# Kernel optimization log

Hardware: AMD Instinct MI355X
Metric: run time of the kernel (lower is better)

## Reference

```python
import jax, jax.numpy as jnp
import numpy as np

N = 50000        # nodes
N_EDGES = 800000 # edges before self loops
D_IN = 128       # in_features
D_OUT = 64       # out_features (per head)
H = 2            # heads
NEG_SLOPE = 0.2  # GATv2Conv default negative_slope
EPS = 1e-5       # LayerNorm eps


def setup_inputs() -> dict:
    key = jax.random.key(0)
    ks = jax.random.split(key, 8)
    X = jax.random.normal(ks[0], (N, D_IN), jnp.float32)
    E = jax.random.randint(ks[1], (2, N_EDGES), 0, N, dtype=jnp.int32)
    attr = jax.random.normal(ks[2], (N_EDGES,), jnp.float32)
    # GATv2Conv params: lin_l / lin_r (share_weights=False, bias=True), att, concat bias
    s_in = 1.0 / np.sqrt(D_IN)
    W_l = jax.random.normal(ks[3], (D_IN, H * D_OUT), jnp.float32) * s_in
    b_l = jnp.zeros((H * D_OUT,), jnp.float32)
    W_r = jax.random.normal(ks[4], (D_IN, H * D_OUT), jnp.float32) * s_in
    b_r = jnp.zeros((H * D_OUT,), jnp.float32)
    att = jax.random.normal(ks[5], (H, D_OUT), jnp.float32) * (1.0 / np.sqrt(D_OUT))
    bias = jnp.zeros((H * D_OUT,), jnp.float32)
    # final_linear + LayerNorm params
    W_f = jax.random.normal(ks[6], (H * D_OUT, D_OUT), jnp.float32) * (1.0 / np.sqrt(H * D_OUT))
    b_f = jnp.zeros((D_OUT,), jnp.float32)
    gamma = jnp.ones((D_OUT,), jnp.float32)
    beta = jnp.zeros((D_OUT,), jnp.float32)
    return dict(X=X, E=E, attr=attr, W_l=W_l, b_l=b_l, W_r=W_r, b_r=b_r,
                att=att, bias=bias, W_f=W_f, b_f=b_f, gamma=gamma, beta=beta)


def _forward(X, E, W_l, b_l, W_r, b_r, att, bias, W_f, b_f, gamma, beta):
    # add self loops (PyG GATv2Conv default add_self_loops=True)
    loop = jnp.arange(N, dtype=E.dtype)
    src = jnp.concatenate([E[0], loop])  # [Et]
    dst = jnp.concatenate([E[1], loop])  # [Et]
    x_l = (X @ W_l + b_l).reshape(N, H, D_OUT)  # source-side transform
    x_r = (X @ W_r + b_r).reshape(N, H, D_OUT)  # target-side transform
    # per-edge GATv2 score: a^T LeakyReLU(x_i + x_j)
    s = jax.nn.leaky_relu(x_l[src] + x_r[dst], NEG_SLOPE)      # [Et, H, C]
    alpha = jnp.einsum('ehc,hc->eh', s, att)                   # [Et, H]
    # segment softmax over incoming edges of each target node
    a_max = jax.ops.segment_max(alpha, dst, num_segments=N)    # [N, H]
    a_max = jnp.where(jnp.isfinite(a_max), a_max, 0.0)
    num = jnp.exp(alpha - a_max[dst])
    den = jax.ops.segment_sum(num, dst, num_segments=N)
    w = num / den[dst]                                         # [Et, H]
    # weighted scatter-aggregate of source messages
    out = jax.ops.segment_sum(x_l[src] * w[:, :, None], dst, num_segments=N)  # [N,H,C]
    out = out.reshape(N, H * D_OUT) + bias                     # concat heads + bias
    # final linear + LayerNorm
    h = out @ W_f + b_f                                        # [N, D_OUT]
    mu = jnp.mean(h, axis=-1, keepdims=True)
    var = jnp.mean((h - mu) ** 2, axis=-1, keepdims=True)
    return (h - mu) * jax.lax.rsqrt(var + EPS) * gamma + beta


def reference(X, E, attr, W_l, b_l, W_r, b_r, att, bias, W_f, b_f, gamma, beta):
    H_out = _forward(X, E, W_l, b_l, W_r, b_r, att, bias, W_f, b_f, gamma, beta)
    return (H_out, E, attr)
```

## Files before the change

kernel.cpp:

```cpp
#include <hip/hip_runtime.h>

typedef unsigned short u16;
typedef unsigned int   u32;


#define DIN   128
#define DOUT  64
#define HD    128
#define BCAP  64

typedef __attribute__((ext_vector_type(8))) _Float16 f16x8;
typedef __attribute__((ext_vector_type(2))) _Float16 h2;
typedef __attribute__((ext_vector_type(4))) float    f32x4;

union H2U { u32 u; h2 h; };
__device__ __forceinline__ h2  U2H(u32 u) { H2U x; x.u = u; return x.h; }
__device__ __forceinline__ u32 H2Ub(h2 h) { H2U x; x.h = h; return x.u; }

__device__ __forceinline__ u16 f2h(float f) {
    _Float16 h = (_Float16)f;
    u16 r; __builtin_memcpy(&r, &h, 2); return r;
}

__device__ __forceinline__ u32 pkmax(u32 a, u32 b) {
    u32 d;
    asm("v_pk_max_f16 %0, %1, %2" : "=v"(d) : "v"(a), "v"(b));
    return d;
}

__device__ __forceinline__ float fdot2f(h2 a, h2 b, float c) {
#if __has_builtin(__builtin_amdgcn_fdot2)
    return __builtin_amdgcn_fdot2(a, b, c, false);
#else
    return c + (float)a[0] * (float)b[0] + (float)a[1] * (float)b[1];
#endif
}

__global__ void prep_small(const float* __restrict__ Wl, const float* __restrict__ Wr,
                           const float* __restrict__ Wf,
                           u16* __restrict__ WTl, u16* __restrict__ WTr,
                           uint4* __restrict__ Wfp, int* __restrict__ count, int N)
{
    int i = blockIdx.x * 256 + threadIdx.x;
    if (i < N) { count[i] = 0; return; }
    int j = i - N;
    if (j < 16384) {
        int k = j >> 7, c = j & 127;
        WTl[c * 128 + k] = f2h(Wl[j]);
    } else if (j < 32768) {
        int t = j - 16384;
        int k = t >> 7, c = t & 127;
        WTr[c * 128 + k] = f2h(Wr[t]);
    } else if (j < 33792) {
        int t = j - 32768;
        int k4 = t >> 5, c = t & 31;
        const float* wrow = Wf + (size_t)(4 * k4) * DOUT;
        u32 a0 = (u32)f2h(wrow[c])              | ((u32)f2h(wrow[DOUT + c]) << 16);
        u32 a1 = (u32)f2h(wrow[2 * DOUT + c])   | ((u32)f2h(wrow[3 * DOUT + c]) << 16);
        u32 a2 = (u32)f2h(wrow[c + 32])         | ((u32)f2h(wrow[DOUT + c + 32]) << 16);
        u32 a3 = (u32)f2h(wrow[2 * DOUT + c + 32]) | ((u32)f2h(wrow[3 * DOUT + c + 32]) << 16);
        Wfp[t] = make_uint4(a0, a1, a2, a3);
    }
}

__global__ __launch_bounds__(256) void gemm_scatter(
    const float* __restrict__ X,
    const u16* __restrict__ WTl, const float* __restrict__ bl,
    const u16* __restrict__ WTr, const float* __restrict__ br,
    const int* __restrict__ E, const float* __restrict__ attr,
    int* __restrict__ count, u16* __restrict__ bucket,
    u16* __restrict__ xl_p, u16* __restrict__ xr_p,
    float* __restrict__ out, int N, int NE)
{
    __shared__ u16 sX[64 * 136];
    __shared__ u16 sW[128 * 136];

    const int tid  = threadIdx.x;
    const int bid  = blockIdx.x;
    const int nB   = gridDim.x;
    const int cb   = bid & 1;
    const int row0 = (bid >> 1) * 64;
    const u16*   WT  = (cb == 0) ? WTl : WTr;
    const float* bia = (cb == 0) ? bl : br;

    {
        int e0 = (int)(((long long)bid) * NE / nB);
        int e1 = (int)(((long long)bid + 1) * NE / nB);
        for (int e = e0 + tid; e < e1; e += 256) {
            int src = E[e];
            int dst = E[NE + e];
            if ((u32)dst >= (u32)N) dst = 0;
            if ((u32)src >= (u32)N) src = 0;
            int rank = atomicAdd(&count[dst], 1);
            if (rank < BCAP) bucket[(size_t)dst * BCAP + rank] = (u16)src;
        }
        const size_t base = (size_t)N * DOUT;
        long long P = 3LL * NE;
        int p0 = (int)(((long long)bid) * P / nB);
        int p1 = (int)(((long long)bid + 1) * P / nB);
        for (int p = p0 + tid; p < p1; p += 256) {
            if (p < 2 * NE) out[base + p] = (float)E[p];
            else            out[base + p] = attr[p - 2 * NE];
        }
    }

    for (int idx = tid; idx < 64 * 32; idx += 256) {
        int r  = idx >> 5;
        int k4 = (idx & 31) << 2;
        int gr = row0 + r;
        float4 v = make_float4(0.f, 0.f, 0.f, 0.f);
        if (gr < N) v = *(const float4*)(X + (size_t)gr * DIN + k4);
        u32 p0 = (u32)f2h(v.x) | ((u32)f2h(v.y) << 16);
        u32 p1 = (u32)f2h(v.z) | ((u32)f2h(v.w) << 16);
        *(uint2*)&sX[r * 136 + k4] = make_uint2(p0, p1);
    }
    for (int idx = tid; idx < 128 * 16; idx += 256) {
        int c  = idx >> 4;
        int k8 = (idx & 15) << 3;
        *(uint4*)&sW[c * 136 + k8] = *(const uint4*)&WT[c * 128 + k8];
    }
    __syncthreads();

    const int wv   = tid >> 6;
    const int lane = tid & 63;
    const int m    = lane & 15;
    const int quad = lane >> 4;

    f32x4 acc[8] = {};
    #pragma unroll
    for (int kc = 0; kc < 4; kc++) {
        f16x8 bx = *(const f16x8*)&sX[(wv * 16 + m) * 136 + kc * 32 + quad * 8];
        #pragma unroll
        for (int t = 0; t < 8; t++) {
            f16x8 aw = *(const f16x8*)&sW[(t * 16 + m) * 136 + kc * 32 + quad * 8];
            acc[t] = __builtin_amdgcn_mfma_f32_16x16x32_f16(aw, bx, acc[t], 0, 0, 0);
        }
    }

    const int gn = row0 + wv * 16 + m;
    if (gn < N) {
        u16* dst = (cb == 0) ? xl_p : xr_p;
        #pragma unroll
        for (int t = 0; t < 8; t++) {
            const int c0 = t * 16 + quad * 4;
            float4 bv = *(const float4*)(bia + c0);
            u32 p0 = (u32)f2h(acc[t][0] + bv.x) | ((u32)f2h(acc[t][1] + bv.y) << 16);
            u32 p1 = (u32)f2h(acc[t][2] + bv.z) | ((u32)f2h(acc[t][3] + bv.w) << 16);
            *(uint2*)(dst + (size_t)gn * HD + c0) = make_uint2(p0, p1);
        }
    }
}

template<int D>
__device__ __forceinline__ void edge_block(
    int myidx, int j, int sgbase, const char* xbase,
    const h2* xr2, const h2* at2, h2 c02,
    h2* acc2, float& lden)
{
    uint4 q[D];
    #pragma unroll
    for (int b = 0; b < D; b++) {
        u32 off = (u32)__shfl(myidx, sgbase + j + 2 * b) << 8;
        q[b] = *(const uint4*)(xbase + off);
    }
    float sh[D];
    #pragma unroll
    for (int b = 0; b < D; b++) {
        h2 v0 = U2H(q[b].x) + xr2[0];
        h2 v1 = U2H(q[b].y) + xr2[1];
        h2 v2 = U2H(q[b].z) + xr2[2];
        h2 v3 = U2H(q[b].w) + xr2[3];
        v0 = U2H(pkmax(H2Ub(v0), H2Ub(v0 * c02)));
        v1 = U2H(pkmax(H2Ub(v1), H2Ub(v1 * c02)));
        v2 = U2H(pkmax(H2Ub(v2), H2Ub(v2 * c02)));
        v3 = U2H(pkmax(H2Ub(v3), H2Ub(v3 * c02)));
        float s = fdot2f(v0, at2[0], 0.f);
        s = fdot2f(v1, at2[1], s);
        s = fdot2f(v2, at2[2], s);
        s = fdot2f(v3, at2[3], s);
        sh[b] = s;
    }
    #pragma unroll
    for (int m = 4; m; m >>= 1) {
        #pragma unroll
        for (int b = 0; b < D; b++) sh[b] += __shfl_xor(sh[b], m);
    }
    #pragma unroll
    for (int b = 0; b < D; b++) {
        float p = exp2f(sh[b]);
        lden += p;
        _Float16 ph = (_Float16)p;
        h2 p2 = {ph, ph};
        acc2[0] += p2 * U2H(q[b].x);
        acc2[1] += p2 * U2H(q[b].y);
        acc2[2] += p2 * U2H(q[b].z);
        acc2[3] += p2 * U2H(q[b].w);
    }
}

__global__ __launch_bounds__(256, 6) void edge_fused(
    const u16* __restrict__ xl_p, const u16* __restrict__ xr_p,
    const float* __restrict__ att, const float* __restrict__ bias,
    const uint4* __restrict__ Wfp, const float* __restrict__ bf,
    const float* __restrict__ gamma, const float* __restrict__ beta,
    const int* __restrict__ count, const u16* __restrict__ bucket,
    float* __restrict__ out, int N)
{
    __shared__ uint4 sWp[32 * 32];
    __shared__ u32   sAggU[8 * 64];

    const int tid = threadIdx.x;
    for (int idx = tid; idx < 1024; idx += 256) sWp[idx] = Wfp[idx];
    __syncthreads();

    const int l      = tid & 63;
    const int half   = tid >> 5;
    const int hl     = tid & 31;
    const int g16    = l & 15;
    const int ch0    = g16 * 8;
    const int sgsel  = (l >> 4) & 1;
    const int sgbase = (l & 32) + sgsel;
    const int n      = blockIdx.x * 8 + half;
    const bool active = (n < N);

    const h2 c02 = {(_Float16)0.2f, (_Float16)0.2f};
    h2 at2[4], xr2[4];
    {
        const float L2E = 1.44269504f;
        float4 a0 = *(const float4*)(att + ch0);
        float4 a1 = *(const float4*)(att + ch0 + 4);
        at2[0] = h2{(_Float16)(a0.x * L2E), (_Float16)(a0.y * L2E)};
        at2[1] = h2{(_Float16)(a0.z * L2E), (_Float16)(a0.w * L2E)};
        at2[2] = h2{(_Float16)(a1.x * L2E), (_Float16)(a1.y * L2E)};
        at2[3] = h2{(_Float16)(a1.z * L2E), (_Float16)(a1.w * L2E)};
        uint4 pr = make_uint4(0, 0, 0, 0);
        if (active) pr = *(const uint4*)(xr_p + (size_t)n * HD + ch0);
        xr2[0] = U2H(pr.x); xr2[1] = U2H(pr.y);
        xr2[2] = U2H(pr.z); xr2[3] = U2H(pr.w);
    }

    h2 acc2[4] = {};
    float lden = 0.f;

    int cnt_b = 0;
    if (active) {
        cnt_b = count[n];
        if (cnt_b < 0) cnt_b = 0;
        if (cnt_b > BCAP) cnt_b = BCAP;
    }
    const int cnt = active ? cnt_b + 1 : 0;
    const u16* mybkt = bucket + (size_t)(active ? n : 0) * BCAP;

    const char* xbase = (const char*)xl_p + ch0 * 2;

    int done = 0;
    while (done < cnt) {
        int chunk = cnt - done; if (chunk > 32) chunk = 32;
        int myidx = 0;
        if (hl < chunk) {
            int gj = done + hl;
            myidx = (gj < cnt_b) ? (int)mybkt[gj] : n;
        }
        int j = 0;
        for (; j + 16 <= chunk; j += 16)
            edge_block<8>(myidx, j, sgbase, xbase, xr2, at2, c02, acc2, lden);
        if (j + 8 <= chunk) {
            edge_block<4>(myidx, j, sgbase, xbase, xr2, at2, c02, acc2, lden);
            j += 8;
        }
        if (j + 4 <= chunk) {
            edge_block<2>(myidx, j, sgbase, xbase, xr2, at2, c02, acc2, lden);
            j += 4;
        }
        for (; j < chunk; j += 2) {
            u32 off = (u32)__shfl(myidx, sgbase + j) << 8;
            uint4 q = *(const uint4*)(xbase + off);
            h2 v0 = U2H(q.x) + xr2[0];
            h2 v1 = U2H(q.y) + xr2[1];
            h2 v2 = U2H(q.z) + xr2[2];
            h2 v3 = U2H(q.w) + xr2[3];
            v0 = U2H(pkmax(H2Ub(v0), H2Ub(v0 * c02)));
            v1 = U2H(pkmax(H2Ub(v1), H2Ub(v1 * c02)));
            v2 = U2H(pkmax(H2Ub(v2), H2Ub(v2 * c02)));
            v3 = U2H(pkmax(H2Ub(v3), H2Ub(v3 * c02)));
            float s = fdot2f(v0, at2[0], 0.f);
            s = fdot2f(v1, at2[1], s);
            s = fdot2f(v2, at2[2], s);
            s = fdot2f(v3, at2[3], s);
            #pragma unroll
            for (int m = 4; m; m >>= 1) s += __shfl_xor(s, m);
            float p = (j + sgsel < chunk) ? exp2f(s) : 0.f;
            lden += p;
            _Float16 ph = (_Float16)p;
            h2 p2 = {ph, ph};
            acc2[0] += p2 * U2H(q.x);
            acc2[1] += p2 * U2H(q.y);
            acc2[2] += p2 * U2H(q.z);
            acc2[3] += p2 * U2H(q.w);
        }
        done += chunk;
    }

    #pragma unroll
    for (int i = 0; i < 4; i++) {
        u32 o = (u32)__shfl_xor((int)H2Ub(acc2[i]), 16);
        acc2[i] = acc2[i] + U2H(o);
    }
    lden += __shfl_xor(lden, 16);

    float rl = 1.f / fmaxf(lden, 1e-30f);
    if (!(l & 16)) {
        float4 b0 = *(const float4*)(bias + ch0);
        float4 b1 = *(const float4*)(bias + ch0 + 4);
        uint4 w;
        w.x = (u32)f2h((float)acc2[0][0] * rl + b0.x) |
              ((u32)f2h((float)acc2[0][1] * rl + b0.y) << 16);
        w.y = (u32)f2h((float)acc2[1][0] * rl + b0.z) |
              ((u32)f2h((float)acc2[1][1] * rl + b0.w) << 16);
        w.z = (u32)f2h((float)acc2[2][0] * rl + b1.x) |
              ((u32)f2h((float)acc2[2][1] * rl + b1.y) << 16);
        w.w = (u32)f2h((float)acc2[3][0] * rl + b1.z) |
              ((u32)f2h((float)acc2[3][1] * rl + b1.w) << 16);
        *(uint4*)&sAggU[half * 64 + g16 * 4] = w;
    }
    asm volatile("s_waitcnt lgkmcnt(0)" ::: "memory");

    float h0 = bf[hl], h1 = bf[hl + 32];
    #pragma unroll 8
    for (int k4 = 0; k4 < 32; k4++) {
        uint4 wp = sWp[k4 * 32 + hl];
        uint2 ag = *(const uint2*)&sAggU[half * 64 + k4 * 2];
        h0 = fdot2f(U2H(ag.x), U2H(wp.x), h0);
        h0 = fdot2f(U2H(ag.y), U2H(wp.y), h0);
        h1 = fdot2f(U2H(ag.x), U2H(wp.z), h1);
        h1 = fdot2f(U2H(ag.y), U2H(wp.w), h1);
    }

    float s1r = h0 + h1, s2r = h0 * h0 + h1 * h1;
    #pragma unroll
    for (int m = 16; m; m >>= 1) { s1r += __shfl_xor(s1r, m); s2r += __shfl_xor(s2r, m); }
    float mu  = s1r * (1.f / 64.f);
    float var = s2r * (1.f / 64.f) - mu * mu;
    float rs  = rsqrtf(fmaxf(var, 0.f) + 1e-5f);
    if (active) {
        out[(size_t)n * DOUT + hl]      = (h0 - mu) * rs * gamma[hl]      + beta[hl];
        out[(size_t)n * DOUT + hl + 32] = (h1 - mu) * rs * gamma[hl + 32] + beta[hl + 32];
    }
}

extern "C" void kernel_launch(void* const* d_in, const int* in_sizes, int n_in,
                              void* d_out, int out_size, void* d_ws, size_t ws_size,
                              hipStream_t stream) {
    const float* X    = (const float*)d_in[0];
    const int*   E    = (const int*)d_in[1];
    const float* attr = (const float*)d_in[2];
    const float* Wl   = (const float*)d_in[3];
    const float* bl   = (const float*)d_in[4];
    const float* Wr   = (const float*)d_in[5];
    const float* br   = (const float*)d_in[6];
    const float* att  = (const float*)d_in[7];
    const float* bias = (const float*)d_in[8];
    const float* Wf   = (const float*)d_in[9];
    const float* bf   = (const float*)d_in[10];
    const float* gamma= (const float*)d_in[11];
    const float* beta = (const float*)d_in[12];
    float* out = (float*)d_out;

    const int N  = in_sizes[0] / DIN;
    const int NE = in_sizes[1] / 2;
    const int GB = (N + 63) / 64;

    char* ws = (char*)d_ws;
    int* count      = (int*)ws;               ws += (size_t)N * 4;
    u16* bucket     = (u16*)ws;               ws += (size_t)N * BCAP * 2;
    u16* xl_p       = (u16*)ws;               ws += (size_t)N * HD * 2;
    u16* xr_p       = (u16*)ws;               ws += (size_t)N * HD * 2;
    u16* WTl        = (u16*)ws;               ws += 128 * 128 * 2;
    u16* WTr        = (u16*)ws;               ws += 128 * 128 * 2;
    uint4* Wfp      = (uint4*)ws;             ws += 1024 * 16;

    prep_small<<<(N + 33792 + 255) / 256, 256, 0, stream>>>(
        Wl, Wr, Wf, WTl, WTr, Wfp, count, N);

    gemm_scatter<<<2 * GB, 256, 0, stream>>>(
        X, WTl, bl, WTr, br, E, attr, count, bucket, xl_p, xr_p, out, N, NE);

    edge_fused<<<(N + 7) / 8, 256, 0, stream>>>(
        xl_p, xr_p, att, bias, Wfp, bf, gamma, beta,
        count, bucket, out, N);
}
```

Measured before the change: 215.8 us.

## Fuse all stages into one persistent cooperative kernel with grid syncs

Replaces the three kernel launches with a single persistent cooperative kernel sized to occupancy. The prep, GEMM/scatter and edge-aggregation stages are separated by grid-wide syncs. The GEMM now reads weights directly from global memory instead of staging them in LDS, and shared memory is overlaid through a union. Odd and even blocks order the GEMM and scatter work differently so the atomics overlap with MFMA work. This removes launch gaps and tail effects, at the risk of lower occupancy in the edge phase and the cost of the grid barriers. A three-kernel fallback is kept in case the cooperative launch fails.

```diff
diff --git a/kernel.cpp b/kernel.cpp
--- a/kernel.cpp
+++ b/kernel.cpp
@@ -1,4 +1,7 @@
 #include <hip/hip_runtime.h>
+#include <hip/hip_cooperative_groups.h>
+
+namespace cg = cooperative_groups;
 
 typedef unsigned short u16;
 typedef unsigned int   u32;
@@ -36,12 +39,16 @@
 #endif
 }
 
-__global__ void prep_small(const float* __restrict__ Wl, const float* __restrict__ Wr,
-                           const float* __restrict__ Wf,
-                           u16* __restrict__ WTl, u16* __restrict__ WTr,
-                           uint4* __restrict__ Wfp, int* __restrict__ count, int N)
-{
-    int i = blockIdx.x * 256 + threadIdx.x;
+union SharedU {
+    u16 sX[64 * 136];
+    struct { uint4 sWp[1024]; u32 sAggU[8 * 64]; } ef;
+};
+
+__device__ __forceinline__ void dev_prep_item(
+    int i, const float* __restrict__ Wl, const float* __restrict__ Wr,
+    const float* __restrict__ Wf, u16* __restrict__ WTl, u16* __restrict__ WTr,
+    uint4* __restrict__ Wfp, int* __restrict__ count, int N)
+{
     if (i < N) { count[i] = 0; return; }
     int j = i - N;
     if (j < 16384) {
@@ -63,47 +70,39 @@
     }
 }
 
-__global__ __launch_bounds__(256) void gemm_scatter(
+__device__ __forceinline__ void dev_scatter_edge(
+    int e, const int* __restrict__ E, int* __restrict__ count,
+    u16* __restrict__ bucket, int N, int NE)
+{
+    int src = E[e];
+    int dst = E[NE + e];
+    if ((u32)dst >= (u32)N) dst = 0;
+    if ((u32)src >= (u32)N) src = 0;
+    int rank = atomicAdd(&count[dst], 1);
+    if (rank < BCAP) bucket[(size_t)dst * BCAP + rank] = (u16)src;
+}
+
+__device__ __forceinline__ void dev_pass_item(
+    int p, const int* __restrict__ E, const float* __restrict__ attr,
+    float* __restrict__ out, size_t base, int NE)
+{
+    if (p < 2 * NE) out[base + p] = (float)E[p];
+    else            out[base + p] = attr[p - 2 * NE];
+}
+
+__device__ __forceinline__ void dev_gemm_tile(
+    int bt, int tid, u16* sX,
     const float* __restrict__ X,
     const u16* __restrict__ WTl, const float* __restrict__ bl,
     const u16* __restrict__ WTr, const float* __restrict__ br,
-    const int* __restrict__ E, const float* __restrict__ attr,
-    int* __restrict__ count, u16* __restrict__ bucket,
-    u16* __restrict__ xl_p, u16* __restrict__ xr_p,
-    float* __restrict__ out, int N, int NE)
-{
-    __shared__ u16 sX[64 * 136];
-    __shared__ u16 sW[128 * 136];
-
-    const int tid  = threadIdx.x;
-    const int bid  = blockIdx.x;
-    const int nB   = gridDim.x;
-    const int cb   = bid & 1;
-    const int row0 = (bid >> 1) * 64;
-    const u16*   WT  = (cb == 0) ? WTl : WTr;
-    const float* bia = (cb == 0) ? bl : br;
-
-    {
-        int e0 = (int)(((long long)bid) * NE / nB);
-        int e1 = (int)(((long long)bid + 1) * NE / nB);
-        for (int e = e0 + tid; e < e1; e += 256) {
-            int src = E[e];
-            int dst = E[NE + e];
-            if ((u32)dst >= (u32)N) dst = 0;
-            if ((u32)src >= (u32)N) src = 0;
-            int rank = atomicAdd(&count[dst], 1);
-            if (rank < BCAP) bucket[(size_t)dst * BCAP + rank] = (u16)src;
-        }
-        const size_t base = (size_t)N * DOUT;
-        long long P = 3LL * NE;
-        int p0 = (int)(((long long)bid) * P / nB);
-        int p1 = (int)(((long long)bid + 1) * P / nB);
-        for (int p = p0 + tid; p < p1; p += 256) {
-            if (p < 2 * NE) out[base + p] = (float)E[p];
-            else            out[base + p] = attr[p - 2 * NE];
-        }
-    }
-
+    u16* __restrict__ xl_p, u16* __restrict__ xr_p, int N)
+{
+    const int cb   = bt & 1;
+    const int row0 = (bt >> 1) * 64;
+    const u16*   WT  = cb ? WTr : WTl;
+    const float* bia = cb ? br : bl;
+
+    __syncthreads();
     for (int idx = tid; idx < 64 * 32; idx += 256) {
         int r  = idx >> 5;
         int k4 = (idx & 31) << 2;
@@ -114,11 +113,6 @@
         u32 p1 = (u32)f2h(v.z) | ((u32)f2h(v.w) << 16);
         *(uint2*)&sX[r * 136 + k4] = make_uint2(p0, p1);
     }
-    for (int idx = tid; idx < 128 * 16; idx += 256) {
-        int c  = idx >> 4;
-        int k8 = (idx & 15) << 3;
-        *(uint4*)&sW[c * 136 + k8] = *(const uint4*)&WT[c * 128 + k8];
-    }
     __syncthreads();
 
     const int wv   = tid >> 6;
@@ -132,14 +126,14 @@
         f16x8 bx = *(const f16x8*)&sX[(wv * 16 + m) * 136 + kc * 32 + quad * 8];
         #pragma unroll
         for (int t = 0; t < 8; t++) {
-            f16x8 aw = *(const f16x8*)&sW[(t * 16 + m) * 136 + kc * 32 + quad * 8];
+            f16x8 aw = *(const f16x8*)&WT[(t * 16 + m) * 128 + kc * 32 + quad * 8];
             acc[t] = __builtin_amdgcn_mfma_f32_16x16x32_f16(aw, bx, acc[t], 0, 0, 0);
         }
     }
 
     const int gn = row0 + wv * 16 + m;
     if (gn < N) {
-        u16* dst = (cb == 0) ? xl_p : xr_p;
+        u16* dst = cb ? xr_p : xl_p;
         #pragma unroll
         for (int t = 0; t < 8; t++) {
             const int c0 = t * 16 + quad * 4;
@@ -198,21 +192,14 @@
     }
 }
 
-__global__ __launch_bounds__(256, 6) void edge_fused(
+__device__ __forceinline__ void dev_edge_group(
+    int g, int tid, const uint4* sWp, u32* sAggU,
     const u16* __restrict__ xl_p, const u16* __restrict__ xr_p,
     const float* __restrict__ att, const float* __restrict__ bias,
-    const uint4* __restrict__ Wfp, const float* __restrict__ bf,
-    const float* __restrict__ gamma, const float* __restrict__ beta,
-    const int* __restrict__ count, const u16* __restrict__ bucket,
-    float* __restrict__ out, int N)
-{
-    __shared__ uint4 sWp[32 * 32];
-    __shared__ u32   sAggU[8 * 64];
-
-    const int tid = threadIdx.x;
-    for (int idx = tid; idx < 1024; idx += 256) sWp[idx] = Wfp[idx];
-    __syncthreads();
-
+    const float* __restrict__ bf, const float* __restrict__ gamma,
+    const float* __restrict__ beta, const int* __restrict__ count,
+    const u16* __restrict__ bucket, float* __restrict__ out, int N)
+{
     const int l      = tid & 63;
     const int half   = tid >> 5;
     const int hl     = tid & 31;
@@ -220,7 +207,7 @@
     const int ch0    = g16 * 8;
     const int sgsel  = (l >> 4) & 1;
     const int sgbase = (l & 32) + sgsel;
-    const int n      = blockIdx.x * 8 + half;
+    const int n      = g * 8 + half;
     const bool active = (n < N);
 
     const h2 c02 = {(_Float16)0.2f, (_Float16)0.2f};
@@ -348,6 +335,108 @@
     }
 }
 
+__global__ __launch_bounds__(256) void fused_all(
+    const float* X, const int* E, const float* attr,
+    const float* Wl, const float* bl, const float* Wr, const float* br,
+    const float* att, const float* bias, const float* Wf, const float* bf,
+    const float* gamma, const float* beta,
+    int* count, u16* bucket, u16* xl_p, u16* xr_p,
+    u16* WTl, u16* WTr, uint4* Wfp, float* out,
+    int N, int NE, int GB)
+{
+    __shared__ SharedU sh;
+    const int tid  = threadIdx.x;
+    const int bid  = blockIdx.x;
+    const int nB   = gridDim.x;
+    const int gsz  = nB * 256;
+    const int gtid = bid * 256 + tid;
+
+    for (int i = gtid; i < N + 33792; i += gsz)
+        dev_prep_item(i, Wl, Wr, Wf, WTl, WTr, Wfp, count, N);
+
+    cg::this_grid().sync();
+
+    const int TT = 2 * GB;
+    if (bid & 1) {
+        for (int bt = bid; bt < TT; bt += nB)
+            dev_gemm_tile(bt, tid, sh.sX, X, WTl, bl, WTr, br, xl_p, xr_p, N);
+        for (int e = gtid; e < NE; e += gsz)
+            dev_scatter_edge(e, E, count, bucket, N, NE);
+    } else {
+        for (int e = gtid; e < NE; e += gsz)
+            dev_scatter_edge(e, E, count, bucket, N, NE);
+        for (int bt = bid; bt < TT; bt += nB)
+            dev_gemm_tile(bt, tid, sh.sX, X, WTl, bl, WTr, br, xl_p, xr_p, N);
+    }
+    {
+        const size_t base = (size_t)N * DOUT;
+        for (int p = gtid; p < 3 * NE; p += gsz)
+            dev_pass_item(p, E, attr, out, base, NE);
+    }
+
+    cg::this_grid().sync();
+
+    for (int idx = tid; idx < 1024; idx += 256) sh.ef.sWp[idx] = Wfp[idx];
+    __syncthreads();
+    const int ngroups = (N + 7) / 8;
+    for (int g = bid; g < ngroups; g += nB)
+        dev_edge_group(g, tid, sh.ef.sWp, sh.ef.sAggU,
+                       xl_p, xr_p, att, bias, bf, gamma, beta,
+                       count, bucket, out, N);
+}
+
+__global__ void k_prep(const float* __restrict__ Wl, const float* __restrict__ Wr,
+                       const float* __restrict__ Wf, u16* __restrict__ WTl,
+                       u16* __restrict__ WTr, uint4* __restrict__ Wfp,
+                       int* __restrict__ count, int N)
+{
+    int i = blockIdx.x * 256 + threadIdx.x;
+    if (i < N + 33792) dev_prep_item(i, Wl, Wr, Wf, WTl, WTr, Wfp, count, N);
+}
+
+__global__ __launch_bounds__(256) void k_work(
+    const float* X, const int* E, const float* attr,
+    const u16* WTl, const float* bl, const u16* WTr, const float* br,
+    int* count, u16* bucket, u16* xl_p, u16* xr_p, float* out,
+    int N, int NE, int GB)
+{
+    __shared__ SharedU sh;
+    const int tid  = threadIdx.x;
+    const int bid  = blockIdx.x;
+    const int nB   = gridDim.x;
+    const int gsz  = nB * 256;
+    const int gtid = bid * 256 + tid;
+    const int TT = 2 * GB;
+    if (bid & 1) {
+        for (int bt = bid; bt < TT; bt += nB)
+            dev_gemm_tile(bt, tid, sh.sX, X, WTl, bl, WTr, br, xl_p, xr_p, N);
+        for (int e = gtid; e < NE; e += gsz)
+            dev_scatter_edge(e, E, count, bucket, N, NE);
+    } else {
+        for (int e = gtid; e < NE; e += gsz)
+            dev_scatter_edge(e, E, count, bucket, N, NE);
+        for (int bt = bid; bt < TT; bt += nB)
+            dev_gemm_tile(bt, tid, sh.sX, X, WTl, bl, WTr, br, xl_p, xr_p, N);
+    }
+    const size_t base = (size_t)N * DOUT;
+    for (int p = gtid; p < 3 * NE; p += gsz)
+        dev_pass_item(p, E, attr, out, base, NE);
+}
+
+__global__ __launch_bounds__(256, 6) void k_edge(
+    const u16* xl_p, const u16* xr_p, const float* att, const float* bias,
+    const uint4* Wfp, const float* bf, const float* gamma, const float* beta,
+    const int* count, const u16* bucket, float* out, int N)
+{
+    __shared__ uint4 sWp[1024];
+    __shared__ u32   sAggU[8 * 64];
+    const int tid = threadIdx.x;
+    for (int idx = tid; idx < 1024; idx += 256) sWp[idx] = Wfp[idx];
+    __syncthreads();
+    dev_edge_group(blockIdx.x, tid, sWp, sAggU, xl_p, xr_p, att, bias,
+                   bf, gamma, beta, count, bucket, out, N);
+}
+
 extern "C" void kernel_launch(void* const* d_in, const int* in_sizes, int n_in,
                               void* d_out, int out_size, void* d_ws, size_t ws_size,
                               hipStream_t stream) {
@@ -366,9 +455,9 @@
     const float* beta = (const float*)d_in[12];
     float* out = (float*)d_out;
 
-    const int N  = in_sizes[0] / DIN;
-    const int NE = in_sizes[1] / 2;
-    const int GB = (N + 63) / 64;
+    int N  = in_sizes[0] / DIN;
+    int NE = in_sizes[1] / 2;
+    int GB = (N + 63) / 64;
 
     char* ws = (char*)d_ws;
     int* count      = (int*)ws;               ws += (size_t)N * 4;
@@ -379,13 +468,45 @@
     u16* WTr        = (u16*)ws;               ws += 128 * 128 * 2;
     uint4* Wfp      = (uint4*)ws;             ws += 1024 * 16;
 
-    prep_small<<<(N + 33792 + 255) / 256, 256, 0, stream>>>(
-        Wl, Wr, Wf, WTl, WTr, Wfp, count, N);
-
-    gemm_scatter<<<2 * GB, 256, 0, stream>>>(
-        X, WTl, bl, WTr, br, E, attr, count, bucket, xl_p, xr_p, out, N, NE);
-
-    edge_fused<<<(N + 7) / 8, 256, 0, stream>>>(
-        xl_p, xr_p, att, bias, Wfp, bf, gamma, beta,
-        count, bucket, out, N);
-}
+    static int coopGrid = -2;
+    if (coopGrid == -2) {
+        int maxB = 0;
+        if (hipOccupancyMaxActiveBlocksPerMultiprocessor(
+                &maxB, (const void*)fused_all, 256, 0) == hipSuccess && maxB > 0) {
+            int dev = 0;
+            hipGetDevice(&dev);
+            hipDeviceProp_t prop{};
+            int nCU = 256;
+            if (hipGetDeviceProperties(&prop, dev) == hipSuccess &&
+                prop.multiProcessorCount > 0)
+                nCU = prop.multiProcessorCount;
+            coopGrid = maxB * nCU;
+        } else {
+            coopGrid = -1;
+        }
+    }
+
+    bool done = false;
+    if (coopGrid > 0) {
+        void* args[] = {
+            (void*)&X, (void*)&E, (void*)&attr,
+            (void*)&Wl, (void*)&bl, (void*)&Wr, (void*)&br,
+            (void*)&att, (void*)&bias, (void*)&Wf, (void*)&bf,
+            (void*)&gamma, (void*)&beta,
+            (void*)&count, (void*)&bucket, (void*)&xl_p, (void*)&xr_p,
+            (void*)&WTl, (void*)&WTr, (void*)&Wfp, (void*)&out,
+            (void*)&N, (void*)&NE, (void*)&GB };
+        if (hipLaunchCooperativeKernel((const void*)fused_all,
+                dim3(coopGrid), dim3(256), args, 0, stream) == hipSuccess)
+            done = true;
+    }
+
+    if (!done) {
+        k_prep<<<(N + 33792 + 255) / 256, 256, 0, stream>>>(
+            Wl, Wr, Wf, WTl, WTr, Wfp, count, N);
+        k_work<<<2 * GB, 256, 0, stream>>>(
+            X, E, attr, WTl, bl, WTr, br, count, bucket, xl_p, xr_p, out, N, NE, GB);
+        k_edge<<<(N + 7) / 8, 256, 0, stream>>>(
+            xl_p, xr_p, att, bias, Wfp, bf, gamma, beta, count, bucket, out, N);
+    }
+}
```

Result: slower. 392.6 us (+81.9%).
